# Performance work log

Measured on AMD Instinct MI355X. Metric: run time of the kernel, lower is better.

## Reference

```python
import jax, jax.numpy as jnp
import numpy as np

B, NV, NRINGS, NDIRS, C, F = 2, 20000, 8, 8, 16, 16


def setup_inputs() -> dict:
    key = jax.random.key(0)
    ks = jax.random.split(key, 7)
    y = jax.random.normal(ks[0], (B, NV, NDIRS, C), jnp.float32)
    contributors = jax.random.randint(ks[1], (NV, NRINGS, NDIRS, 3), 0, NV, dtype=jnp.int32)
    weights_bary = jax.random.uniform(ks[2], (NV, NRINGS, NDIRS, 3), jnp.float32)
    angles = jax.random.randint(ks[3], (NV, NRINGS, NDIRS, 3), 0, NDIRS, dtype=jnp.int32)
    kernel = jax.random.normal(ks[4], (NRINGS, NDIRS, C, F), jnp.float32) * 0.05
    center_kernel = jax.random.normal(ks[5], (C, F), jnp.float32) * 0.05
    bias = jnp.zeros((F,), jnp.float32)
    return {"y": y, "contributors": contributors, "weights_bary": weights_bary,
            "angles": angles, "kernel": kernel, "center_kernel": center_kernel, "bias": bias}


def reference(y, contributors, weights_bary, angles, kernel, center_kernel, bias):
    # y: (B, nv, ndirs, C); tables: (nv, nrings, ndirs, 3)
    b, nv, ndirs, nch = y.shape
    nfilters = kernel.shape[-1]
    nrings = contributors.shape[1]

    # window_interpolation_sync: gather 3 contributor vertices per window bin,
    # with the direction axis re-indexed per-contributor (radial sync), then
    # barycentric-weighted sum.  Flatten (vertex, dir) into one gather index.
    idx = contributors * ndirs + angles                 # (nv, nrings, ndirs, 3)
    y_flat = y.reshape(b, nv * ndirs, nch)
    gathered = y_flat[:, idx, :]                        # (B, nv, nrings, ndirs, 3, C)
    z = jnp.einsum('bvrdjc,vrdj->bvrdc', gathered, weights_bary)  # (B, nv, nrings, ndirs, C)

    # gcnn_conv: circular pad over dirs then VALID conv with (nrings, ndirs) kernel
    zr = z.reshape(b * nv, nrings, ndirs, nch)
    zr = jnp.concatenate([zr, zr[:, :, :-1, :]], axis=2)  # width 2*ndirs-1
    conv = jax.lax.conv_general_dilated(
        zr, kernel, window_strides=(1, 1), padding='VALID',
        dimension_numbers=('NHWC', 'HWIO', 'NHWC'))       # (B*nv, 1, ndirs, F)
    conv = conv.reshape(b, nv, ndirs, nfilters)

    out = conv + jnp.einsum('bvdc,cf->bvdf', y, center_kernel) + bias
    out = jax.nn.relu(out)
    return jnp.max(out, axis=2)                          # take_max over directions -> (B, nv, F)
```

## Files before the change

### kernel.cpp

```cpp
#include <hip/hip_runtime.h>

typedef unsigned short u16;
typedef __attribute__((ext_vector_type(4))) unsigned int u32x4;
typedef __attribute__((ext_vector_type(4))) float f32x4;
typedef __attribute__((ext_vector_type(8))) __bf16 bf16x8;

constexpr int BATCH = 2;
constexpr int NV    = 20000;
constexpr int ND    = 8;
constexpr int CH    = 16;
constexpr int NF    = 16;
constexpr int NVD   = NV * ND;
constexpr int K0    = 1024;
constexpr int KE    = 1152;
constexpr int NCHUNK = KE / 32;
constexpr int MTOT  = BATCH * NV;
constexpr int BSTR  = 40;

constexpr size_t Y16_OFF_B = 0;
constexpr size_t K2C_OFF_B = 10240000;
constexpr size_t ZC_OFF_B  = 10534912;

__device__ __forceinline__ u16 f2bf(float x) {
    unsigned int u = __float_as_uint(x);
    unsigned int r = (u + 0x7fffu + ((u >> 16) & 1u)) >> 16;
    return (u16)r;
}
__device__ __forceinline__ unsigned int pack2bf(float a, float b) {
    return (unsigned int)f2bf(a) | ((unsigned int)f2bf(b) << 16);
}

__global__ __launch_bounds__(256) void prep(const float* __restrict__ y,
                                            u16* __restrict__ y16,
                                            u16* __restrict__ zc) {
    int tid = blockIdx.x * 256 + threadIdx.x;
    const float4* src = (const float4*)(y + (size_t)tid * 16);
    float4 v0 = src[0], v1 = src[1], v2 = src[2], v3 = src[3];
    u32x4 lo = {pack2bf(v0.x, v0.y), pack2bf(v0.z, v0.w), pack2bf(v1.x, v1.y), pack2bf(v1.z, v1.w)};
    u32x4 hi = {pack2bf(v2.x, v2.y), pack2bf(v2.z, v2.w), pack2bf(v3.x, v3.y), pack2bf(v3.z, v3.w)};
    u16* yd = y16 + (size_t)tid * 16;
    *(u32x4*)(yd)     = lo;
    *(u32x4*)(yd + 8) = hi;
    int iv = tid >> 3, d = tid & 7;
    u16* zd = zc + ((size_t)(32 + (d >> 1)) * MTOT + iv) * 32 + (d & 1) * 16;
    *(u32x4*)(zd)     = lo;
    *(u32x4*)(zd + 8) = hi;
}

__global__ __launch_bounds__(256) void k2_build(const float* __restrict__ kern,
                                                const float* __restrict__ ck,
                                                u16* __restrict__ k2c) {
    int e = blockIdx.x * 256 + threadIdx.x;
    int i = e & 4095;
    int kc = e >> 12;
    int n = i >> 5, kk = i & 31;
    int k = kc * 32 + kk;
    int w = n >> 4, f = n & 15;
    float val;
    if (k < K0) {
        int r = k >> 7, dd = (k >> 4) & 7, c = k & 15;
        int d = (dd - w) & 7;
        val = kern[((r * 8 + d) * 16 + c) * 16 + f];
    } else {
        int ke = k - K0;
        int d = ke >> 4, c = ke & 15;
        val = (d == w) ? ck[c * 16 + f] : 0.f;
    }
    k2c[e] = f2bf(val);
}

__global__ __launch_bounds__(256) void gather(const u16* __restrict__ y16,
                                              const int* __restrict__ contrib,
                                              const float* __restrict__ wbary,
                                              const int* __restrict__ angles,
                                              u16* __restrict__ zc) {
    int item = blockIdx.x * 256 + threadIdx.x;
    int iv = item >> 6, rd = item & 63;
    int b = iv >= NV;
    int v = iv - b * NV;
    size_t mb = ((size_t)v * 64 + rd) * 3;
    const u16* ybase = y16 + (size_t)b * NVD * CH;

    float acc[CH];
    #pragma unroll
    for (int c = 0; c < CH; ++c) acc[c] = 0.f;
    #pragma unroll
    for (int j = 0; j < 3; ++j) {
        int cn = contrib[mb + j];
        int an = angles[mb + j];
        float wj = wbary[mb + j];
        const u16* src = ybase + ((size_t)cn * ND + an) * CH;
        u32x4 p0 = *(const u32x4*)(src);
        u32x4 p1 = *(const u32x4*)(src + 8);
        #pragma unroll
        for (int q = 0; q < 4; ++q) {
            unsigned int u = p0[q];
            acc[2 * q]     += wj * __uint_as_float(u << 16);
            acc[2 * q + 1] += wj * __uint_as_float(u & 0xffff0000u);
        }
        #pragma unroll
        for (int q = 0; q < 4; ++q) {
            unsigned int u = p1[q];
            acc[8 + 2 * q]     += wj * __uint_as_float(u << 16);
            acc[8 + 2 * q + 1] += wj * __uint_as_float(u & 0xffff0000u);
        }
    }
    u32x4 o0, o1;
    #pragma unroll
    for (int q = 0; q < 4; ++q) {
        o0[q] = pack2bf(acc[2 * q], acc[2 * q + 1]);
        o1[q] = pack2bf(acc[8 + 2 * q], acc[8 + 2 * q + 1]);
    }
    u16* dst = zc + ((size_t)(rd >> 1) * MTOT + iv) * 32 + (rd & 1) * 16;
    *(u32x4*)(dst)     = o0;
    *(u32x4*)(dst + 8) = o1;
}

__global__ __launch_bounds__(256) void gemm_max(const u16* __restrict__ zc,
                                                const u16* __restrict__ k2c,
                                                const float* __restrict__ bias,
                                                float* __restrict__ out) {
    __shared__ __align__(16) u16 Bb[2][128 * BSTR];
    const int t = threadIdx.x;
    const int w = t >> 6, lane = t & 63;
    const int lrow = lane & 15, lq = lane >> 4;
    const int m0 = blockIdx.x * 64;
    const int arow = m0 + w * 16 + lrow;

    const int sn = t >> 1, sh = (t & 1) * 16;

    {
        const u32x4* src = (const u32x4*)(k2c + (size_t)0 * 4096 + sn * 32 + sh);
        u32x4 b0 = src[0], b1 = src[1];
        u16* dst = &Bb[0][sn * BSTR + sh];
        *(u32x4*)(dst)     = b0;
        *(u32x4*)(dst + 8) = b1;
    }
    bf16x8 a_next = *(const bf16x8*)(zc + ((size_t)0 * MTOT + arow) * 32 + lq * 8);

    f32x4 acc[8];
    #pragma unroll
    for (int nt = 0; nt < 8; ++nt) acc[nt] = (f32x4){0.f, 0.f, 0.f, 0.f};

    for (int kc = 0; kc < NCHUNK; ++kc) {
        __syncthreads();
        bf16x8 a = a_next;
        u32x4 bn0, bn1;
        if (kc < NCHUNK - 1) {
            a_next = *(const bf16x8*)(zc + ((size_t)(kc + 1) * MTOT + arow) * 32 + lq * 8);
            const u32x4* src = (const u32x4*)(k2c + (size_t)(kc + 1) * 4096 + sn * 32 + sh);
            bn0 = src[0]; bn1 = src[1];
        }
        bf16x8 bf[8];
        #pragma unroll
        for (int nt = 0; nt < 8; ++nt)
            bf[nt] = *(const bf16x8*)(&Bb[kc & 1][(nt * 16 + lrow) * BSTR + lq * 8]);
        #pragma unroll
        for (int nt = 0; nt < 8; ++nt)
            acc[nt] = __builtin_amdgcn_mfma_f32_16x16x32_bf16(a, bf[nt], acc[nt], 0, 0, 0);
        if (kc < NCHUNK - 1) {
            u16* dst = &Bb[(kc + 1) & 1][sn * BSTR + sh];
            *(u32x4*)(dst)     = bn0;
            *(u32x4*)(dst + 8) = bn1;
        }
    }

    const float bb = bias[lrow];
    #pragma unroll
    for (int reg = 0; reg < 4; ++reg) {
        float m = 0.f;
        #pragma unroll
        for (int nt = 0; nt < 8; ++nt) m = fmaxf(m, acc[nt][reg] + bb);
        out[((size_t)(m0 + w * 16 + lq * 4 + reg)) * NF + lrow] = m;
    }
}

extern "C" void kernel_launch(void* const* d_in, const int* in_sizes, int n_in,
                              void* d_out, int out_size, void* d_ws, size_t ws_size,
                              hipStream_t stream) {
    const float* y      = (const float*)d_in[0];
    const int*   contrib= (const int*)d_in[1];
    const float* wbary  = (const float*)d_in[2];
    const int*   angles = (const int*)d_in[3];
    const float* kern   = (const float*)d_in[4];
    const float* ck     = (const float*)d_in[5];
    const float* bias   = (const float*)d_in[6];
    float* out = (float*)d_out;

    u16* y16 = (u16*)((char*)d_ws + Y16_OFF_B);
    u16* k2c = (u16*)((char*)d_ws + K2C_OFF_B);
    u16* zc  = (u16*)((char*)d_ws + ZC_OFF_B);

    prep<<<1250, 256, 0, stream>>>(y, y16, zc);
    k2_build<<<(NCHUNK * 4096) / 256, 256, 0, stream>>>(kern, ck, k2c);
    gather<<<10000, 256, 0, stream>>>(y16, contrib, wbary, angles, zc);
    gemm_max<<<MTOT / 64, 256, 0, stream>>>(zc, k2c, bias, out);
}
```

Baseline: 215.4 us.

## Fuse barycentric gather into MFMA GEMM, removing the zc intermediate buffer

Removes the separate gather kernel and the zc workspace. The GEMM kernel now builds each A fragment in registers by gathering three bf16 contributor rows and blending them with the barycentric weights. Metadata loads, gathers and B-tile loads are software-pipelined two to three chunks ahead to hide the latency of the irregular loads. This saves writing and re-reading the interpolated tensor, at the cost of more registers, less occupancy, and gather latency now sitting on the GEMM critical path.

Result: slower. 299.3 us (+38.9%).

```diff
diff --git a/kernel.cpp b/kernel.cpp
--- a/kernel.cpp
+++ b/kernel.cpp
@@ -11,15 +11,12 @@
 constexpr int CH    = 16;
 constexpr int NF    = 16;
 constexpr int NVD   = NV * ND;
-constexpr int K0    = 1024;
-constexpr int KE    = 1152;
-constexpr int NCHUNK = KE / 32;
+constexpr int NCHUNK = 36;
 constexpr int MTOT  = BATCH * NV;
 constexpr int BSTR  = 40;
 
 constexpr size_t Y16_OFF_B = 0;
 constexpr size_t K2C_OFF_B = 10240000;
-constexpr size_t ZC_OFF_B  = 10534912;
 
 __device__ __forceinline__ u16 f2bf(float x) {
     unsigned int u = __float_as_uint(x);
@@ -31,8 +28,7 @@
 }
 
 __global__ __launch_bounds__(256) void prep(const float* __restrict__ y,
-                                            u16* __restrict__ y16,
-                                            u16* __restrict__ zc) {
+                                            u16* __restrict__ y16) {
     int tid = blockIdx.x * 256 + threadIdx.x;
     const float4* src = (const float4*)(y + (size_t)tid * 16);
     float4 v0 = src[0], v1 = src[1], v2 = src[2], v3 = src[3];
@@ -41,10 +37,6 @@
     u16* yd = y16 + (size_t)tid * 16;
     *(u32x4*)(yd)     = lo;
     *(u32x4*)(yd + 8) = hi;
-    int iv = tid >> 3, d = tid & 7;
-    u16* zd = zc + ((size_t)(32 + (d >> 1)) * MTOT + iv) * 32 + (d & 1) * 16;
-    *(u32x4*)(zd)     = lo;
-    *(u32x4*)(zd + 8) = hi;
 }
 
 __global__ __launch_bounds__(256) void k2_build(const float* __restrict__ kern,
@@ -57,78 +49,87 @@
     int k = kc * 32 + kk;
     int w = n >> 4, f = n & 15;
     float val;
-    if (k < K0) {
+    if (k < 1024) {
         int r = k >> 7, dd = (k >> 4) & 7, c = k & 15;
         int d = (dd - w) & 7;
         val = kern[((r * 8 + d) * 16 + c) * 16 + f];
     } else {
-        int ke = k - K0;
+        int ke = k - 1024;
         int d = ke >> 4, c = ke & 15;
         val = (d == w) ? ck[c * 16 + f] : 0.f;
     }
     k2c[e] = f2bf(val);
 }
 
-__global__ __launch_bounds__(256) void gather(const u16* __restrict__ y16,
-                                              const int* __restrict__ contrib,
-                                              const float* __restrict__ wbary,
-                                              const int* __restrict__ angles,
-                                              u16* __restrict__ zc) {
-    int item = blockIdx.x * 256 + threadIdx.x;
-    int iv = item >> 6, rd = item & 63;
-    int b = iv >= NV;
-    int v = iv - b * NV;
-    size_t mb = ((size_t)v * 64 + rd) * 3;
-    const u16* ybase = y16 + (size_t)b * NVD * CH;
-
-    float acc[CH];
-    #pragma unroll
-    for (int c = 0; c < CH; ++c) acc[c] = 0.f;
-    #pragma unroll
-    for (int j = 0; j < 3; ++j) {
-        int cn = contrib[mb + j];
-        int an = angles[mb + j];
-        float wj = wbary[mb + j];
-        const u16* src = ybase + ((size_t)cn * ND + an) * CH;
-        u32x4 p0 = *(const u32x4*)(src);
-        u32x4 p1 = *(const u32x4*)(src + 8);
-        #pragma unroll
-        for (int q = 0; q < 4; ++q) {
-            unsigned int u = p0[q];
-            acc[2 * q]     += wj * __uint_as_float(u << 16);
-            acc[2 * q + 1] += wj * __uint_as_float(u & 0xffff0000u);
-        }
-        #pragma unroll
-        for (int q = 0; q < 4; ++q) {
-            unsigned int u = p1[q];
-            acc[8 + 2 * q]     += wj * __uint_as_float(u << 16);
-            acc[8 + 2 * q + 1] += wj * __uint_as_float(u & 0xffff0000u);
-        }
-    }
-    u32x4 o0, o1;
-    #pragma unroll
-    for (int q = 0; q < 4; ++q) {
-        o0[q] = pack2bf(acc[2 * q], acc[2 * q + 1]);
-        o1[q] = pack2bf(acc[8 + 2 * q], acc[8 + 2 * q + 1]);
-    }
-    u16* dst = zc + ((size_t)(rd >> 1) * MTOT + iv) * 32 + (rd & 1) * 16;
-    *(u32x4*)(dst)     = o0;
-    *(u32x4*)(dst + 8) = o1;
-}
-
-__global__ __launch_bounds__(256) void gemm_max(const u16* __restrict__ zc,
-                                                const u16* __restrict__ k2c,
-                                                const float* __restrict__ bias,
-                                                float* __restrict__ out) {
+__global__ __launch_bounds__(256) void fused_gather_gemm(const u16* __restrict__ y16,
+                                                         const int* __restrict__ contrib,
+                                                         const float* __restrict__ wbary,
+                                                         const int* __restrict__ angles,
+                                                         const u16* __restrict__ k2c,
+                                                         const float* __restrict__ bias,
+                                                         float* __restrict__ out) {
     __shared__ __align__(16) u16 Bb[2][128 * BSTR];
     const int t = threadIdx.x;
     const int w = t >> 6, lane = t & 63;
     const int lrow = lane & 15, lq = lane >> 4;
+    const int s_p = lq >> 1;
+    const int h8  = (lq & 1) * 8;
     const int m0 = blockIdx.x * 64;
     const int arow = m0 + w * 16 + lrow;
-
+    const int b_p = (arow >= NV);
+    const int v_p = arow - b_p * NV;
+    const u16* __restrict__ yb = y16 + (size_t)b_p * NVD * CH + h8;
+    const int mb0 = v_p * 192 + s_p * 3;
     const int sn = t >> 1, sh = (t & 1) * 16;
 
+    u32x4 G[2][3];
+    int   mc[2][3], ma[2][3];
+    float mw[2][3], W[2][3];
+    u32x4 bn[2][2];
+
+    f32x4 acc[8];
+    #pragma unroll
+    for (int nt = 0; nt < 8; ++nt) acc[nt] = (f32x4){0.f, 0.f, 0.f, 0.f};
+
+#define META_ISSUE(KC) { const int P_ = (KC) & 1; const int o_ = mb0 + (KC) * 6;       \
+    mc[P_][0] = contrib[o_]; mc[P_][1] = contrib[o_ + 1]; mc[P_][2] = contrib[o_ + 2]; \
+    ma[P_][0] = angles[o_];  ma[P_][1] = angles[o_ + 1];  ma[P_][2] = angles[o_ + 2];  \
+    mw[P_][0] = wbary[o_];   mw[P_][1] = wbary[o_ + 1];   mw[P_][2] = wbary[o_ + 2]; }
+
+#define G_ISSUE(KC) { const int P_ = (KC) & 1;                                          \
+    if ((KC) < 32) {                                                                    \
+        _Pragma("unroll")                                                               \
+        for (int j_ = 0; j_ < 3; ++j_) {                                                \
+            G[P_][j_] = *(const u32x4*)(yb + (size_t)((unsigned)mc[P_][j_] * 128u +     \
+                                                      (unsigned)ma[P_][j_] * 16u));     \
+            W[P_][j_] = mw[P_][j_];                                                     \
+        }                                                                               \
+    } else {                                                                            \
+        G[P_][0] = *(const u32x4*)(yb + (size_t)((unsigned)v_p * 128u +                 \
+                                                 (unsigned)(2 * ((KC) - 32) + s_p) * 16u)); \
+    } }
+
+#define COMBINE(KC, A_) { const int P_ = (KC) & 1;                                      \
+    if ((KC) < 32) {                                                                    \
+        float ac_[8];                                                                   \
+        _Pragma("unroll") for (int x_ = 0; x_ < 8; ++x_) ac_[x_] = 0.f;                 \
+        _Pragma("unroll")                                                               \
+        for (int j_ = 0; j_ < 3; ++j_) {                                                \
+            float wj_ = W[P_][j_];                                                      \
+            _Pragma("unroll")                                                           \
+            for (int q_ = 0; q_ < 4; ++q_) {                                            \
+                unsigned u_ = G[P_][j_][q_];                                            \
+                ac_[2 * q_]     += wj_ * __uint_as_float(u_ << 16);                     \
+                ac_[2 * q_ + 1] += wj_ * __uint_as_float(u_ & 0xffff0000u);             \
+            }                                                                           \
+        }                                                                               \
+        u32x4 o_;                                                                       \
+        _Pragma("unroll") for (int q_ = 0; q_ < 4; ++q_)                                \
+            o_[q_] = pack2bf(ac_[2 * q_], ac_[2 * q_ + 1]);                             \
+        A_ = *(bf16x8*)&o_;                                                             \
+    } else { u32x4 o_ = G[P_][0]; A_ = *(bf16x8*)&o_; } }
+
+    META_ISSUE(0); META_ISSUE(1);
     {
         const u32x4* src = (const u32x4*)(k2c + (size_t)0 * 4096 + sn * 32 + sh);
         u32x4 b0 = src[0], b1 = src[1];
@@ -136,21 +137,24 @@
         *(u32x4*)(dst)     = b0;
         *(u32x4*)(dst + 8) = b1;
     }
-    bf16x8 a_next = *(const bf16x8*)(zc + ((size_t)0 * MTOT + arow) * 32 + lq * 8);
-
-    f32x4 acc[8];
+    G_ISSUE(0); META_ISSUE(2);
+    G_ISSUE(1);
+    {
+        const u32x4* src = (const u32x4*)(k2c + (size_t)1 * 4096 + sn * 32 + sh);
+        bn[1][0] = src[0]; bn[1][1] = src[1];
+    }
+
     #pragma unroll
-    for (int nt = 0; nt < 8; ++nt) acc[nt] = (f32x4){0.f, 0.f, 0.f, 0.f};
-
     for (int kc = 0; kc < NCHUNK; ++kc) {
         __syncthreads();
-        bf16x8 a = a_next;
-        u32x4 bn0, bn1;
-        if (kc < NCHUNK - 1) {
-            a_next = *(const bf16x8*)(zc + ((size_t)(kc + 1) * MTOT + arow) * 32 + lq * 8);
-            const u32x4* src = (const u32x4*)(k2c + (size_t)(kc + 1) * 4096 + sn * 32 + sh);
-            bn0 = src[0]; bn1 = src[1];
+        if (kc + 2 < NCHUNK) {
+            const u32x4* src = (const u32x4*)(k2c + (size_t)(kc + 2) * 4096 + sn * 32 + sh);
+            bn[kc & 1][0] = src[0]; bn[kc & 1][1] = src[1];
         }
+        bf16x8 a;
+        COMBINE(kc, a);
+        if (kc + 2 < NCHUNK) G_ISSUE(kc + 2);
+        if (kc + 3 < 32)     META_ISSUE(kc + 3);
         bf16x8 bf[8];
         #pragma unroll
         for (int nt = 0; nt < 8; ++nt)
@@ -158,12 +162,15 @@
         #pragma unroll
         for (int nt = 0; nt < 8; ++nt)
             acc[nt] = __builtin_amdgcn_mfma_f32_16x16x32_bf16(a, bf[nt], acc[nt], 0, 0, 0);
-        if (kc < NCHUNK - 1) {
+        if (kc + 1 < NCHUNK) {
             u16* dst = &Bb[(kc + 1) & 1][sn * BSTR + sh];
-            *(u32x4*)(dst)     = bn0;
-            *(u32x4*)(dst + 8) = bn1;
+            *(u32x4*)(dst)     = bn[(kc + 1) & 1][0];
+            *(u32x4*)(dst + 8) = bn[(kc + 1) & 1][1];
         }
     }
+#undef META_ISSUE
+#undef G_ISSUE
+#undef COMBINE
 
     const float bb = bias[lrow];
     #pragma unroll
@@ -189,10 +196,9 @@
 
     u16* y16 = (u16*)((char*)d_ws + Y16_OFF_B);
     u16* k2c = (u16*)((char*)d_ws + K2C_OFF_B);
-    u16* zc  = (u16*)((char*)d_ws + ZC_OFF_B);
-
-    prep<<<1250, 256, 0, stream>>>(y, y16, zc);
+
+    prep<<<1250, 256, 0, stream>>>(y, y16);
     k2_build<<<(NCHUNK * 4096) / 256, 256, 0, stream>>>(kern, ck, k2c);
-    gather<<<10000, 256, 0, stream>>>(y16, contrib, wbary, angles, zc);
-    gemm_max<<<MTOT / 64, 256, 0, stream>>>(zc, k2c, bias, out);
-}
+    fused_gather_gemm<<<MTOT / 64, 256, 0, stream>>>(y16, contrib, wbary, angles,
+                                                     k2c, bias, out);
+}
```
